# Kernel tuning notes

Hardware: AMD Instinct MI355X
Metric: run time of the kernel (lower is better)

The kernel has to match this reference:

```python
import jax, jax.numpy as jnp
import numpy as np

RRELU_SLOPE = 0.2  # eval-mode RReLU with lower=0.1, upper=0.3 -> (0.1+0.3)/2


def setup_inputs() -> dict:
    key = jax.random.key(0)
    k1, k2, k3 = jax.random.split(key, 3)
    B, C, H, W = 16, 64, 256, 256
    x = jax.random.normal(k1, (B, C, H, W), dtype=jnp.float32)
    mix = jax.random.normal(k2, (C, C), dtype=jnp.float32) / np.sqrt(C)
    bias = jax.random.normal(k3, (C,), dtype=jnp.float32) * 0.1
    return {"x": x, "mix": mix, "bias": bias}


def reference(x, mix, bias):
    # Softmax2d: softmax over channel dim at each spatial location
    s = jax.nn.softmax(x, axis=1)                     # (B,C,H,W)
    # channel mix: out[d] = sum_c mix[d,c] * s[c]  (== s_flat @ mix.T in torch)
    mixed = jnp.einsum('bchw,dc->bdhw', s, mix)
    mixed = mixed + bias[None, :, None, None]
    # RReLU (deterministic eval-mode slope)
    activated = jnp.where(mixed >= 0, mixed, RRELU_SLOPE * mixed)
    out = jax.nn.relu(activated + 0.1 * x)
    return out
```

## Files before the change

kernel.cpp:

```cpp
#include <hip/hip_runtime.h>
#include <math.h>

#define HWSZ 65536

typedef __bf16 bf16x8 __attribute__((ext_vector_type(8)));
typedef __bf16 bf16x4 __attribute__((ext_vector_type(4)));
typedef float f32x4 __attribute__((ext_vector_type(4)));

__global__ __launch_bounds__(256) void cvt_mix_kernel(const float* __restrict__ mix,
                                                      __bf16* __restrict__ mixb) {
    int i = blockIdx.x * 256 + threadIdx.x;
    mixb[i] = (__bf16)mix[i];
}

__global__ __launch_bounds__(256) void fused_kernel(
    const float* __restrict__ x, const __bf16* __restrict__ mixb,
    const float* __restrict__ bias, float* __restrict__ out)
{
    __shared__ __bf16 sT[4][64 * 64];
    const int tid  = threadIdx.x;
    const int wid  = tid >> 6;
    const int lane = tid & 63;
    const int waveg = blockIdx.x * 4 + wid;
    const int b   = waveg >> 10;
    const int hw0 = (waveg & 1023) << 6;
    const size_t ibase = (size_t)b * (64 * HWSZ) + hw0;

    const float LOG2E = 1.44269504088896340736f;
    const float LN2   = 0.69314718055994530942f;

    const float* xp = x + ibase + lane;
    __bf16* my = &sT[wid][0];
    float sA = 0.f, sB = 0.f;
#pragma unroll
    for (int j = 0; j < 8; ++j) {
        float e8[8];
#pragma unroll
        for (int i = 0; i < 8; ++i) e8[i] = xp[(size_t)(j * 8 + i) << 16];
        bf16x8 v;
#pragma unroll
        for (int i = 0; i < 8; ++i) {
            e8[i] = __builtin_exp2f(e8[i] * LOG2E);
            v[i] = (__bf16)e8[i];
        }
        sA += (e8[0] + e8[2]) + (e8[4] + e8[6]);
        sB += (e8[1] + e8[3]) + (e8[5] + e8[7]);
        const int gr = j ^ (lane & 7);
        *reinterpret_cast<bf16x8*>(my + lane * 64 + gr * 8) = v;
    }
    const float inv = 1.f / (sA + sB);
    asm volatile("s_waitcnt lgkmcnt(0)" ::: "memory");

    const int l15 = lane & 15, lhi = lane >> 4;

    float ivp[4];
#pragma unroll
    for (int nt = 0; nt < 4; ++nt)
        ivp[nt] = __shfl(inv, nt * 16 + l15, 64);

#pragma unroll
    for (int mtp = 0; mtp < 2; ++mtp) {
        f32x4 acc[2][4] = {};
#pragma unroll
        for (int kt = 0; kt < 2; ++kt) {
            bf16x8 A[2], B[4];
            const __bf16* ab = mixb + (mtp * 32 + l15) * 64 + kt * 32 + lhi * 8;
#pragma unroll
            for (int mt = 0; mt < 2; ++mt)
                A[mt] = *reinterpret_cast<const bf16x8*>(ab + mt * 16 * 64);
#pragma unroll
            for (int nt = 0; nt < 4; ++nt) {
                const int row = nt * 16 + l15;
                const int g = (kt * 4 + lhi) ^ (row & 7);
                B[nt] = *reinterpret_cast<const bf16x8*>(my + row * 64 + g * 8);
            }
#pragma unroll
            for (int mt = 0; mt < 2; ++mt)
#pragma unroll
                for (int nt = 0; nt < 4; ++nt)
                    acc[mt][nt] = __builtin_amdgcn_mfma_f32_16x16x32_bf16(
                        A[mt], B[nt], acc[mt][nt], 0, 0, 0);
        }

#pragma unroll
        for (int mt = 0; mt < 2; ++mt) {
            const int d0 = mtp * 32 + mt * 16 + lhi * 4;
            const float bb[4] = {bias[d0], bias[d0 + 1], bias[d0 + 2], bias[d0 + 3]};
#pragma unroll
            for (int nt = 0; nt < 4; ++nt) {
                const int p = nt * 16 + l15;
                const int g = ((d0 >> 3) ^ (p & 7));
                const bf16x4 sv = *reinterpret_cast<const bf16x4*>(
                    my + p * 64 + g * 8 + (d0 & 7));
                float* orw = out + ibase + (size_t)d0 * HWSZ + p;
#pragma unroll
                for (int r = 0; r < 4; ++r) {
                    float mixed = fmaf(acc[mt][nt][r], ivp[nt], bb[r]);
                    float act = fmaxf(mixed, 0.2f * mixed);
                    float xv = LN2 * __builtin_log2f((float)sv[r]);
                    float v = fmaf(0.1f, xv, act);
                    orw[(size_t)r * HWSZ] = fmaxf(v, 0.f);
                }
            }
        }
    }
}

extern "C" void kernel_launch(void* const* d_in, const int* in_sizes, int n_in,
                              void* d_out, int out_size, void* d_ws, size_t ws_size,
                              hipStream_t stream) {
    const float* x    = (const float*)d_in[0];
    const float* mix  = (const float*)d_in[1];
    const float* bias = (const float*)d_in[2];
    float* out = (float*)d_out;
    __bf16* mixb = (__bf16*)d_ws;
    (void)in_sizes; (void)n_in; (void)out_size; (void)ws_size;

    cvt_mix_kernel<<<dim3(16), dim3(256), 0, stream>>>(mix, mixb);
    fused_kernel<<<dim3(4096), dim3(256), 0, stream>>>(x, mixb, bias, out);
}
```

Before: 122.6 us.

## Shrink per-wave tile to 16 pixels with channel-split lanes and max-stable softmax

Each wave now handles 16 spatial positions instead of 64. The 64 channels are split across the four lane groups, and the max and sum are reduced with cross-lane shuffles. The softmax values go straight into registers as MFMA B operands, so B is no longer read back from LDS. Mix weights are hoisted into registers once, LDS per wave shrinks, and the grid grows to four times as many blocks for more occupancy and latency hiding. Max subtraction is added for numerical stability, and x is still recovered from the bf16 log. The cost is more redundant A loads across waves, and each lane's loads now cover only 16 contiguous floats.

```diff
diff --git a/kernel.cpp b/kernel.cpp
--- a/kernel.cpp
+++ b/kernel.cpp
@@ -17,91 +17,89 @@
     const float* __restrict__ x, const __bf16* __restrict__ mixb,
     const float* __restrict__ bias, float* __restrict__ out)
 {
-    __shared__ __bf16 sT[4][64 * 64];
+    __shared__ __bf16 sT[4][16 * 64];
     const int tid  = threadIdx.x;
     const int wid  = tid >> 6;
     const int lane = tid & 63;
+    const int l15  = lane & 15, lhi = lane >> 4;
     const int waveg = blockIdx.x * 4 + wid;
-    const int b   = waveg >> 10;
-    const int hw0 = (waveg & 1023) << 6;
-    const size_t ibase = (size_t)b * (64 * HWSZ) + hw0;
+    const int p0 = waveg << 4;
+    const int b  = p0 >> 16;
+    const int hw = p0 & (HWSZ - 1);
+    const size_t ibase = (size_t)b * (64 * HWSZ) + hw;
+    __bf16* my = &sT[wid][0];
 
     const float LOG2E = 1.44269504088896340736f;
     const float LN2   = 0.69314718055994530942f;
 
-    const float* xp = x + ibase + lane;
-    __bf16* my = &sT[wid][0];
+    bf16x8 A[4][2];
+#pragma unroll
+    for (int mt = 0; mt < 4; ++mt)
+#pragma unroll
+        for (int kt = 0; kt < 2; ++kt)
+            A[mt][kt] = *reinterpret_cast<const bf16x8*>(
+                mixb + (mt * 16 + l15) * 64 + kt * 32 + lhi * 8);
+
+    const float* xp = x + ibase + l15;
+    float e8[16];
+#pragma unroll
+    for (int h = 0; h < 2; ++h)
+#pragma unroll
+        for (int i = 0; i < 8; ++i)
+            e8[h * 8 + i] = xp[(size_t)(h * 32 + lhi * 8 + i) << 16];
+
+    float mx = fmaxf(fmaxf(fmaxf(e8[0], e8[1]), fmaxf(e8[2], e8[3])),
+                     fmaxf(fmaxf(e8[4], e8[5]), fmaxf(e8[6], e8[7])));
+    float mx2 = fmaxf(fmaxf(fmaxf(e8[8], e8[9]), fmaxf(e8[10], e8[11])),
+                      fmaxf(fmaxf(e8[12], e8[13]), fmaxf(e8[14], e8[15])));
+    mx = fmaxf(mx, mx2);
+    mx = fmaxf(mx, __shfl_xor(mx, 16, 64));
+    mx = fmaxf(mx, __shfl_xor(mx, 32, 64));
+
     float sA = 0.f, sB = 0.f;
 #pragma unroll
-    for (int j = 0; j < 8; ++j) {
-        float e8[8];
+    for (int i = 0; i < 16; i += 2) {
+        e8[i]     = __builtin_exp2f((e8[i]     - mx) * LOG2E); sA += e8[i];
+        e8[i + 1] = __builtin_exp2f((e8[i + 1] - mx) * LOG2E); sB += e8[i + 1];
+    }
+    float s = sA + sB;
+    s += __shfl_xor(s, 16, 64);
+    s += __shfl_xor(s, 32, 64);
+    const float inv = 1.f / s;
+
+    bf16x8 v0, v1;
 #pragma unroll
-        for (int i = 0; i < 8; ++i) e8[i] = xp[(size_t)(j * 8 + i) << 16];
-        bf16x8 v;
-#pragma unroll
-        for (int i = 0; i < 8; ++i) {
-            e8[i] = __builtin_exp2f(e8[i] * LOG2E);
-            v[i] = (__bf16)e8[i];
-        }
-        sA += (e8[0] + e8[2]) + (e8[4] + e8[6]);
-        sB += (e8[1] + e8[3]) + (e8[5] + e8[7]);
-        const int gr = j ^ (lane & 7);
-        *reinterpret_cast<bf16x8*>(my + lane * 64 + gr * 8) = v;
+    for (int i = 0; i < 8; ++i) { v0[i] = (__bf16)e8[i]; v1[i] = (__bf16)e8[8 + i]; }
+
+    {
+        const int s7 = l15 & 7;
+        *reinterpret_cast<bf16x8*>(my + l15 * 64 + ((lhi    ) ^ s7) * 8) = v0;
+        *reinterpret_cast<bf16x8*>(my + l15 * 64 + ((lhi + 4) ^ s7) * 8) = v1;
     }
-    const float inv = 1.f / (sA + sB);
     asm volatile("s_waitcnt lgkmcnt(0)" ::: "memory");
 
-    const int l15 = lane & 15, lhi = lane >> 4;
-
-    float ivp[4];
+    f32x4 acc[4] = {};
 #pragma unroll
-    for (int nt = 0; nt < 4; ++nt)
-        ivp[nt] = __shfl(inv, nt * 16 + l15, 64);
+    for (int mt = 0; mt < 4; ++mt) {
+        acc[mt] = __builtin_amdgcn_mfma_f32_16x16x32_bf16(A[mt][0], v0, acc[mt], 0, 0, 0);
+        acc[mt] = __builtin_amdgcn_mfma_f32_16x16x32_bf16(A[mt][1], v1, acc[mt], 0, 0, 0);
+    }
 
 #pragma unroll
-    for (int mtp = 0; mtp < 2; ++mtp) {
-        f32x4 acc[2][4] = {};
+    for (int mt = 0; mt < 4; ++mt) {
+        const int d0 = mt * 16 + lhi * 4;
+        const f32x4 bb = *reinterpret_cast<const f32x4*>(bias + d0);
+        const int g = ((mt * 2 + (lhi >> 1)) ^ (l15 & 7));
+        const bf16x4 sv = *reinterpret_cast<const bf16x4*>(
+            my + l15 * 64 + g * 8 + (lhi & 1) * 4);
+        float* orw = out + ibase + (size_t)d0 * HWSZ + l15;
 #pragma unroll
-        for (int kt = 0; kt < 2; ++kt) {
-            bf16x8 A[2], B[4];
-            const __bf16* ab = mixb + (mtp * 32 + l15) * 64 + kt * 32 + lhi * 8;
-#pragma unroll
-            for (int mt = 0; mt < 2; ++mt)
-                A[mt] = *reinterpret_cast<const bf16x8*>(ab + mt * 16 * 64);
-#pragma unroll
-            for (int nt = 0; nt < 4; ++nt) {
-                const int row = nt * 16 + l15;
-                const int g = (kt * 4 + lhi) ^ (row & 7);
-                B[nt] = *reinterpret_cast<const bf16x8*>(my + row * 64 + g * 8);
-            }
-#pragma unroll
-            for (int mt = 0; mt < 2; ++mt)
-#pragma unroll
-                for (int nt = 0; nt < 4; ++nt)
-                    acc[mt][nt] = __builtin_amdgcn_mfma_f32_16x16x32_bf16(
-                        A[mt], B[nt], acc[mt][nt], 0, 0, 0);
-        }
-
-#pragma unroll
-        for (int mt = 0; mt < 2; ++mt) {
-            const int d0 = mtp * 32 + mt * 16 + lhi * 4;
-            const float bb[4] = {bias[d0], bias[d0 + 1], bias[d0 + 2], bias[d0 + 3]};
-#pragma unroll
-            for (int nt = 0; nt < 4; ++nt) {
-                const int p = nt * 16 + l15;
-                const int g = ((d0 >> 3) ^ (p & 7));
-                const bf16x4 sv = *reinterpret_cast<const bf16x4*>(
-                    my + p * 64 + g * 8 + (d0 & 7));
-                float* orw = out + ibase + (size_t)d0 * HWSZ + p;
-#pragma unroll
-                for (int r = 0; r < 4; ++r) {
-                    float mixed = fmaf(acc[mt][nt][r], ivp[nt], bb[r]);
-                    float act = fmaxf(mixed, 0.2f * mixed);
-                    float xv = LN2 * __builtin_log2f((float)sv[r]);
-                    float v = fmaf(0.1f, xv, act);
-                    orw[(size_t)r * HWSZ] = fmaxf(v, 0.f);
-                }
-            }
+        for (int r = 0; r < 4; ++r) {
+            float mixed = fmaf(acc[mt][r], inv, bb[r]);
+            float act = fmaxf(mixed, 0.2f * mixed);
+            float xv = fmaf(LN2, __builtin_log2f((float)sv[r]), mx);
+            float v = fmaf(0.1f, xv, act);
+            orw[(size_t)r * HWSZ] = fmaxf(v, 0.f);
         }
     }
 }
@@ -117,5 +115,5 @@
     (void)in_sizes; (void)n_in; (void)out_size; (void)ws_size;
 
     cvt_mix_kernel<<<dim3(16), dim3(256), 0, stream>>>(mix, mixb);
-    fused_kernel<<<dim3(4096), dim3(256), 0, stream>>>(x, mixb, bias, out);
+    fused_kernel<<<dim3(16384), dim3(256), 0, stream>>>(x, mixb, bias, out);
 }
```

Result: slower. 159.9 us (+30.5%).
